# Performance work log

Hardware: AMD Instinct MI355X
Metric: run time of the kernel (lower is better)

## Reference

```python
import jax, jax.numpy as jnp
import numpy as np

B, N, M = 4, 4096, 4096


def setup_inputs() -> dict:
    key = jax.random.key(0)
    k1, k2 = jax.random.split(key)
    source = jax.random.normal(k1, (B, N, 3), dtype=jnp.float32)
    target = jax.random.normal(k2, (B, M, 3), dtype=jnp.float32)
    return {"source": source, "target": target}


def reference(source, target):
    # Pairwise squared distances: dist[b, n, m] = ||source[b,n] - target[b,m]||^2
    x2 = jnp.sum(source * source, axis=-1)          # (B, N)
    y2 = jnp.sum(target * target, axis=-1)          # (B, M)
    xy = jnp.einsum('bnd,bmd->bnm', source, target)  # (B, N, M)
    dist = x2[:, :, None] + y2[:, None, :] - 2.0 * xy
    # bidirectional Chamfer (default args: bidirectional=True, reverse=False)
    loss_s2t = jnp.mean(jnp.min(dist, axis=2), axis=1)  # (B,)
    loss_t2s = jnp.mean(jnp.min(dist, axis=1), axis=1)  # (B,)
    return jnp.mean(loss_s2t + loss_t2s)
```

## Files before the change

### kernel.cpp

```cpp
#include <hip/hip_runtime.h>

namespace {
constexpr int kB = 4;
constexpr int kN = 4096;
constexpr int kP = 2 * kB * kN;
constexpr int kBlk = 256;
constexpr int kSplit = 16;
constexpr int kChunk = kN / kSplit;
}


__device__ __forceinline__ unsigned enc(float f) {
  unsigned u = __float_as_uint(f);
  return (u & 0x80000000u) ? ~u : (u | 0x80000000u);
}
__device__ __forceinline__ float dec(unsigned k) {
  return __uint_as_float((k & 0x80000000u) ? (k ^ 0x80000000u) : ~k);
}

__global__ __launch_bounds__(kBlk) void cham_prep_kernel(
    const float* __restrict__ src, const float* __restrict__ tgt,
    float4* __restrict__ pack, unsigned int* __restrict__ keys,
    float* __restrict__ out) {
  int i = blockIdx.x * kBlk + threadIdx.x;
  if (i < kP) {
    const float* p = (i < kB * kN) ? (tgt + (size_t)i * 3)
                                   : (src + (size_t)(i - kB * kN) * 3);
    float x = p[0], y = p[1], z = p[2];
    pack[i] = make_float4(x, y, z, fmaf(x, x, fmaf(y, y, z * z)));
    keys[i] = 0xFFFFFFFFu;
  }
  if (i == 0 && blockIdx.x == 0) out[0] = 0.0f;
}

__global__ __launch_bounds__(kBlk) void cham_min_kernel(
    const float4* __restrict__ pack, unsigned int* __restrict__ keys) {
  const int dir = blockIdx.z;
  const int b = blockIdx.y;
  const int chunk = blockIdx.x & (kSplit - 1);
  const int ntile = blockIdx.x / kSplit;
  const int n = ntile * kBlk + threadIdx.x;

  const float4* __restrict__ own = pack + (size_t)(dir ^ 1) * kB * kN;
  const float4* __restrict__ oth = pack + (size_t)dir * kB * kN;

  const float4 v = own[(size_t)b * kN + n];
  const float nx = -2.0f * v.x, ny = -2.0f * v.y, nz = -2.0f * v.z;

  const float4* __restrict__ q = oth + (size_t)b * kN + chunk * kChunk;

  float e0 = 3.4e38f, e1 = 3.4e38f, e2 = 3.4e38f, e3 = 3.4e38f;
#pragma unroll 4
  for (int m = 0; m < kChunk; m += 4) {
    float4 a = q[m + 0];
    float4 bb = q[m + 1];
    float4 c = q[m + 2];
    float4 d = q[m + 3];
    e0 = fminf(e0, fmaf(nx, a.x, fmaf(ny, a.y, fmaf(nz, a.z, a.w))));
    e1 = fminf(e1, fmaf(nx, bb.x, fmaf(ny, bb.y, fmaf(nz, bb.z, bb.w))));
    e2 = fminf(e2, fmaf(nx, c.x, fmaf(ny, c.y, fmaf(nz, c.z, c.w))));
    e3 = fminf(e3, fmaf(nx, d.x, fmaf(ny, d.y, fmaf(nz, d.z, d.w))));
  }

  float best = fminf(fminf(e0, e1), fminf(e2, e3)) + v.w;
  atomicMin(&keys[((size_t)dir * kB + b) * kN + n], enc(best));
}

__global__ __launch_bounds__(kBlk) void cham_reduce_kernel(
    const unsigned int* __restrict__ keys, float* __restrict__ out) {
  __shared__ float red[kBlk];
  float acc = 0.0f;
  for (int i = blockIdx.x * kBlk + threadIdx.x; i < kP; i += gridDim.x * kBlk)
    acc += dec(keys[i]);
  red[threadIdx.x] = acc;
  __syncthreads();
  for (int s = kBlk / 2; s > 0; s >>= 1) {
    if (threadIdx.x < s) red[threadIdx.x] += red[threadIdx.x + s];
    __syncthreads();
  }
  if (threadIdx.x == 0) atomicAdd(out, red[0] * (1.0f / (kB * kN)));
}

extern "C" void kernel_launch(void* const* d_in, const int* in_sizes, int n_in,
                              void* d_out, int out_size, void* d_ws,
                              size_t ws_size, hipStream_t stream) {
  const float* src = (const float*)d_in[0];
  const float* tgt = (const float*)d_in[1];
  float* out = (float*)d_out;

  unsigned int* keys = (unsigned int*)d_ws;
  float4* pack = (float4*)((char*)d_ws + (size_t)kP * 4);

  cham_prep_kernel<<<dim3(kP / kBlk), kBlk, 0, stream>>>(src, tgt, pack, keys,
                                                         out);

  dim3 grid(kN / kBlk * kSplit, kB, 2);
  cham_min_kernel<<<grid, kBlk, 0, stream>>>(pack, keys);

  cham_reduce_kernel<<<dim3(32), kBlk, 0, stream>>>(keys, out);
}
```

Measured before the change: 76.28 us.

## Pack points into paired SoA records, use packed FMA, fuse final reduction

The prep kernel now stores points in 64-byte records that interleave pairs of x/y/z/w values, so the min loop can evaluate two candidates per packed-float2 FMA. The min kernel computes its own point's values directly from the inputs, and the last block to finish (found through an atomic counter and threadfences) does the final sum, which removes the separate reduce kernel launch. This trades one kernel launch for a serialized tail reduction in a single block and extra atomics.

After: 186.3 us. 144% more time.

```diff
diff --git a/kernel.cpp b/kernel.cpp
--- a/kernel.cpp
+++ b/kernel.cpp
@@ -1,14 +1,23 @@
 #include <hip/hip_runtime.h>
+
+typedef float f2 __attribute__((ext_vector_type(2)));
 
 namespace {
 constexpr int kB = 4;
 constexpr int kN = 4096;
-constexpr int kP = 2 * kB * kN;
+constexpr int kPts = kB * kN;
+constexpr int kP = 2 * kPts;
 constexpr int kBlk = 256;
 constexpr int kSplit = 16;
 constexpr int kChunk = kN / kSplit;
+constexpr int kChunkRecs = kChunk / 4;
+constexpr int kGrid = (kN / kBlk) * kSplit * kB * 2;
+constexpr float kInf = 3.4e38f;
 }
 
+struct alignas(64) Rec4 {
+  float4 a, b, c, d;
+};
 
 __device__ __forceinline__ unsigned enc(float f) {
   unsigned u = __float_as_uint(f);
@@ -18,67 +27,91 @@
   return __uint_as_float((k & 0x80000000u) ? (k ^ 0x80000000u) : ~k);
 }
 
+
 __global__ __launch_bounds__(kBlk) void cham_prep_kernel(
     const float* __restrict__ src, const float* __restrict__ tgt,
-    float4* __restrict__ pack, unsigned int* __restrict__ keys,
-    float* __restrict__ out) {
+    float* __restrict__ packf, unsigned* __restrict__ keys,
+    unsigned* __restrict__ counter) {
   int i = blockIdx.x * kBlk + threadIdx.x;
-  if (i < kP) {
-    const float* p = (i < kB * kN) ? (tgt + (size_t)i * 3)
-                                   : (src + (size_t)(i - kB * kN) * 3);
-    float x = p[0], y = p[1], z = p[2];
-    pack[i] = make_float4(x, y, z, fmaf(x, x, fmaf(y, y, z * z)));
-    keys[i] = 0xFFFFFFFFu;
-  }
-  if (i == 0 && blockIdx.x == 0) out[0] = 0.0f;
+  const float* p =
+      (i < kPts) ? (tgt + (size_t)i * 3) : (src + (size_t)(i - kPts) * 3);
+  float x = p[0], y = p[1], z = p[2];
+  float w = fmaf(x, x, fmaf(y, y, z * z));
+  int rec = i >> 2, sub = i & 3;
+  int pair = sub >> 1, k = sub & 1;
+  float* rp = packf + (size_t)rec * 16 + pair * 8 + k;
+  rp[0] = x;
+  rp[2] = y;
+  rp[4] = z;
+  rp[6] = w;
+  keys[i] = 0xFFFFFFFFu;
+  if (i == 0) *counter = 0u;
 }
 
 __global__ __launch_bounds__(kBlk) void cham_min_kernel(
-    const float4* __restrict__ pack, unsigned int* __restrict__ keys) {
+    const float* __restrict__ src, const float* __restrict__ tgt,
+    const Rec4* __restrict__ pack, unsigned* __restrict__ keys,
+    unsigned* __restrict__ counter, float* __restrict__ out) {
   const int dir = blockIdx.z;
   const int b = blockIdx.y;
   const int chunk = blockIdx.x & (kSplit - 1);
-  const int ntile = blockIdx.x / kSplit;
+  const int ntile = blockIdx.x >> 4;
   const int n = ntile * kBlk + threadIdx.x;
 
-  const float4* __restrict__ own = pack + (size_t)(dir ^ 1) * kB * kN;
-  const float4* __restrict__ oth = pack + (size_t)dir * kB * kN;
+  const float* own = dir ? tgt : src;
+  const float* p = own + ((size_t)b * kN + n) * 3;
+  const float x = p[0], y = p[1], z = p[2];
+  const float w = fmaf(x, x, fmaf(y, y, z * z));
+  const f2 NX = {-2.0f * x, -2.0f * x};
+  const f2 NY = {-2.0f * y, -2.0f * y};
+  const f2 NZ = {-2.0f * z, -2.0f * z};
 
-  const float4 v = own[(size_t)b * kN + n];
-  const float nx = -2.0f * v.x, ny = -2.0f * v.y, nz = -2.0f * v.z;
+  const Rec4* __restrict__ q =
+      pack + ((size_t)dir * kB + b) * (kN / 4) + chunk * kChunkRecs;
 
-  const float4* __restrict__ q = oth + (size_t)b * kN + chunk * kChunk;
+  float best0 = kInf, best1 = kInf;
+#pragma unroll 4
+  for (int r = 0; r < kChunkRecs; ++r) {
+    Rec4 rc = q[r];
+    f2 X0 = {rc.a.x, rc.a.y}, Y0 = {rc.a.z, rc.a.w};
+    f2 Z0 = {rc.b.x, rc.b.y}, W0 = {rc.b.z, rc.b.w};
+    f2 e0 = __builtin_elementwise_fma(
+                NX, X0, __builtin_elementwise_fma(NY, Y0, NZ * Z0)) +
+            W0;
+    f2 X1 = {rc.c.x, rc.c.y}, Y1 = {rc.c.z, rc.c.w};
+    f2 Z1 = {rc.d.x, rc.d.y}, W1 = {rc.d.z, rc.d.w};
+    f2 e1 = __builtin_elementwise_fma(
+                NX, X1, __builtin_elementwise_fma(NY, Y1, NZ * Z1)) +
+            W1;
+    best0 = fminf(best0, fminf(e0.x, e0.y));
+    best1 = fminf(best1, fminf(e1.x, e1.y));
+  }
+  const float best = fminf(best0, best1) + w;
+  atomicMin(&keys[((size_t)dir * kB + b) * kN + n], enc(best));
 
-  float e0 = 3.4e38f, e1 = 3.4e38f, e2 = 3.4e38f, e3 = 3.4e38f;
+  __threadfence();
+  __shared__ int lastFlag;
+  if (threadIdx.x == 0)
+    lastFlag = (atomicAdd(counter, 1u) == (unsigned)(kGrid - 1));
+  __syncthreads();
+  if (!lastFlag) return;
+  __threadfence();
+
+  const uint4* __restrict__ k4 = (const uint4*)keys;
+  float acc = 0.0f;
 #pragma unroll 4
-  for (int m = 0; m < kChunk; m += 4) {
-    float4 a = q[m + 0];
-    float4 bb = q[m + 1];
-    float4 c = q[m + 2];
-    float4 d = q[m + 3];
-    e0 = fminf(e0, fmaf(nx, a.x, fmaf(ny, a.y, fmaf(nz, a.z, a.w))));
-    e1 = fminf(e1, fmaf(nx, bb.x, fmaf(ny, bb.y, fmaf(nz, bb.z, bb.w))));
-    e2 = fminf(e2, fmaf(nx, c.x, fmaf(ny, c.y, fmaf(nz, c.z, c.w))));
-    e3 = fminf(e3, fmaf(nx, d.x, fmaf(ny, d.y, fmaf(nz, d.z, d.w))));
+  for (int i = threadIdx.x; i < kP / 4; i += kBlk) {
+    uint4 v = k4[i];
+    acc += (dec(v.x) + dec(v.y)) + (dec(v.z) + dec(v.w));
   }
-
-  float best = fminf(fminf(e0, e1), fminf(e2, e3)) + v.w;
-  atomicMin(&keys[((size_t)dir * kB + b) * kN + n], enc(best));
-}
-
-__global__ __launch_bounds__(kBlk) void cham_reduce_kernel(
-    const unsigned int* __restrict__ keys, float* __restrict__ out) {
   __shared__ float red[kBlk];
-  float acc = 0.0f;
-  for (int i = blockIdx.x * kBlk + threadIdx.x; i < kP; i += gridDim.x * kBlk)
-    acc += dec(keys[i]);
   red[threadIdx.x] = acc;
   __syncthreads();
   for (int s = kBlk / 2; s > 0; s >>= 1) {
     if (threadIdx.x < s) red[threadIdx.x] += red[threadIdx.x + s];
     __syncthreads();
   }
-  if (threadIdx.x == 0) atomicAdd(out, red[0] * (1.0f / (kB * kN)));
+  if (threadIdx.x == 0) out[0] = red[0] * (1.0f / kPts);
 }
 
 extern "C" void kernel_launch(void* const* d_in, const int* in_sizes, int n_in,
@@ -88,14 +121,14 @@
   const float* tgt = (const float*)d_in[1];
   float* out = (float*)d_out;
 
-  unsigned int* keys = (unsigned int*)d_ws;
-  float4* pack = (float4*)((char*)d_ws + (size_t)kP * 4);
+  unsigned* keys = (unsigned*)d_ws;
+  float* packf = (float*)((char*)d_ws + (size_t)kP * 4);
+  unsigned* counter = (unsigned*)((char*)d_ws + (size_t)kP * 4 + (size_t)kP * 16);
 
-  cham_prep_kernel<<<dim3(kP / kBlk), kBlk, 0, stream>>>(src, tgt, pack, keys,
-                                                         out);
+  cham_prep_kernel<<<dim3(kP / kBlk), kBlk, 0, stream>>>(src, tgt, packf, keys,
+                                                         counter);
 
   dim3 grid(kN / kBlk * kSplit, kB, 2);
-  cham_min_kernel<<<grid, kBlk, 0, stream>>>(pack, keys);
-
-  cham_reduce_kernel<<<dim3(32), kBlk, 0, stream>>>(keys, out);
+  cham_min_kernel<<<grid, kBlk, 0, stream>>>(src, tgt, (const Rec4*)packf,
+                                             keys, counter, out);
 }
```
